# Optimization experiments

Measured on AMD Instinct MI355X. Metric: run time of the kernel, lower is better.

Reference implementation:

```python
import jax, jax.numpy as jnp
import numpy as np

B, S = 32, 4096
Q_DIM, KV_DIM, A_DIM = 512, 512, 128


def setup_inputs() -> dict:
    key = jax.random.key(0)
    k1, k2, k3, k4, k5, k6 = jax.random.split(key, 6)
    query = jax.random.normal(k1, (B, Q_DIM), dtype=jnp.float32)
    kv = jax.random.normal(k2, (B, S, KV_DIM), dtype=jnp.float32)
    mask = jax.random.randint(k3, (B, S), 0, 2).astype(bool)
    # learned params (torch Linear(in, out, bias=False) stores W as [out, in]; we apply x @ W.T)
    Wq = jax.random.normal(k4, (A_DIM, Q_DIM), dtype=jnp.float32) / np.sqrt(Q_DIM)
    Wk = jax.random.normal(k5, (A_DIM, KV_DIM), dtype=jnp.float32) / np.sqrt(KV_DIM)
    Ws = jax.random.normal(k6, (1, A_DIM), dtype=jnp.float32) / np.sqrt(A_DIM)
    return {"query": query, "kv": kv, "mask": mask, "Wq": Wq, "Wk": Wk, "Ws": Ws}


def reference(query, kv, mask, Wq, Wk, Ws):
    # q: [B, 1, A], k: [B, S, A]
    q = jnp.einsum('bq,aq->ba', query, Wq)[:, None, :]
    k = jnp.einsum('bsk,ak->bsa', kv, Wk)
    # additive (Bahdanau) scores: [B, S]
    scores = jnp.einsum('bsa,a->bs', jnp.tanh(q + k), Ws[0])
    scores = jnp.where(mask, scores, -jnp.inf)
    weights = jax.nn.softmax(scores, axis=-1)
    context = jnp.einsum('bs,bsk->bk', weights, kv)
    return context, weights
```

## Files before the change

### kernel.cpp

```cpp
#include <hip/hip_runtime.h>


typedef __attribute__((ext_vector_type(8))) short short8;
typedef __attribute__((ext_vector_type(4))) float f32x4;

#define S_LEN 4096
#define BATCH 32
#define KVD 512
#define AD 128
#define SCHN 32
#define CHUNKS_PER_B (S_LEN / SCHN)
#define NCHUNK (BATCH * CHUNKS_PER_B)

#define FLAG_OFF   0
#define Q_OFF      1024
#define WK_OFF     17408
#define SCORES_OFF 148480
#define MD_OFF     672768
#define CTXP_OFF   705536

__device__ __forceinline__ unsigned short f2bf(float f) {
  unsigned int u = __float_as_uint(f);
  u = (u + 0x7FFFu + ((u >> 16) & 1u)) >> 16;
  return (unsigned short)u;
}
__device__ __forceinline__ float tanh_fast(float x) {
  return 1.0f - 2.0f / (1.0f + __expf(2.0f * x));
}
__device__ __forceinline__ short8 pack8(float4 lo, float4 hi) {
  short8 r;
  r[0] = (short)f2bf(lo.x); r[1] = (short)f2bf(lo.y);
  r[2] = (short)f2bf(lo.z); r[3] = (short)f2bf(lo.w);
  r[4] = (short)f2bf(hi.x); r[5] = (short)f2bf(hi.y);
  r[6] = (short)f2bf(hi.z); r[7] = (short)f2bf(hi.w);
  return r;
}

__global__ __launch_bounds__(256) void prep_kernel(
    const float* __restrict__ query, const float* __restrict__ Wq,
    const float* __restrict__ Wk, const void* __restrict__ maskp,
    float* __restrict__ qws, unsigned short* __restrict__ wkb,
    int* __restrict__ flagp) {
  int blk = blockIdx.x, t = threadIdx.x;
  if (blk < 32) {
    __shared__ float qrow[KVD];
    qrow[t] = query[blk * KVD + t];
    qrow[t + 256] = query[blk * KVD + t + 256];
    __syncthreads();
    int a = t >> 1, half = t & 1;
    const float4* wq4 = (const float4*)(Wq + (size_t)a * KVD + half * 256);
    const float4* qr4 = (const float4*)(qrow + half * 256);
    float s = 0.f;
#pragma unroll 8
    for (int i = 0; i < 64; ++i) {
      float4 wv = wq4[i], qv = qr4[i];
      s += wv.x * qv.x + wv.y * qv.y + wv.z * qv.z + wv.w * qv.w;
    }
    s += __shfl_xor(s, 1);
    if (half == 0) qws[blk * AD + a] = s;
  } else if (blk < 40) {
    int j = blk - 32;
    const float4* src = (const float4*)Wk;
#pragma unroll 4
    for (int i = 0; i < 8; ++i) {
      int idx4 = j * 2048 + i * 256 + t;
      float4 v = src[idx4];
      ushort4 o;
      o.x = f2bf(v.x); o.y = f2bf(v.y); o.z = f2bf(v.z); o.w = f2bf(v.w);
      ((ushort4*)wkb)[idx4] = o;
    }
  } else {
    __shared__ int okv;
    if (t == 0) okv = 1;
    __syncthreads();
    if (t < 128) {
      int wv = ((const int*)maskp)[t];
      if (!(wv == 0 || wv == 1)) okv = 0;
    }
    __syncthreads();
    if (t == 0) flagp[0] = okv;
  }
}

__global__ __launch_bounds__(256, 3) void main_kernel(
    const float* __restrict__ kv, const void* __restrict__ maskp,
    const float* __restrict__ Ws, const float* __restrict__ qws,
    const unsigned short* __restrict__ wkb, const int* __restrict__ flagp,
    float* __restrict__ scores, float* __restrict__ md,
    float* __restrict__ ctxp) {
  int t = threadIdx.x;
  int lane = t & 63, wave = t >> 6;
  int g = blockIdx.x * 4 + wave;
  int b = g >> 7, chunk = g & 127;
  int s0 = chunk * SCHN;
  int lr = lane & 15, lg = lane >> 4;

  __shared__ float esc[4][SCHN];
  __shared__ float ssc[4][SCHN];

  const float* arow0 = kv + ((size_t)b * S_LEN + s0 + lr) * KVD + lg * 8;
  const float* arow1 = arow0 + (size_t)16 * KVD;
  const unsigned short* brow = wkb + (size_t)lr * KVD + lg * 8;

  f32x4 acc[2][8];
#pragma unroll
  for (int mi = 0; mi < 2; ++mi)
#pragma unroll
    for (int n = 0; n < 8; ++n) acc[mi][n] = (f32x4)0.f;

  for (int kk = 0; kk < KVD / 32; ++kk) {
    int ko = kk * 32;
    float4 a0lo = *(const float4*)(arow0 + ko);
    float4 a0hi = *(const float4*)(arow0 + ko + 4);
    float4 a1lo = *(const float4*)(arow1 + ko);
    float4 a1hi = *(const float4*)(arow1 + ko + 4);
    short8 bfr[8];
#pragma unroll
    for (int n = 0; n < 8; ++n)
      bfr[n] = *(const short8*)(brow + (size_t)n * 16 * KVD + ko);
    short8 af0 = pack8(a0lo, a0hi);
    short8 af1 = pack8(a1lo, a1hi);
#pragma unroll
    for (int n = 0; n < 8; ++n) {
      acc[0][n] = __builtin_amdgcn_mfma_f32_16x16x32_bf16(af0, bfr[n], acc[0][n], 0, 0, 0);
      acc[1][n] = __builtin_amdgcn_mfma_f32_16x16x32_bf16(af1, bfr[n], acc[1][n], 0, 0, 0);
    }
  }

  float qv[8], wv[8];
#pragma unroll
  for (int n = 0; n < 8; ++n) {
    qv[n] = qws[b * AD + n * 16 + lr];
    wv[n] = Ws[n * 16 + lr];
  }
  int flag = flagp[0];
  float sc[2][4];
#pragma unroll
  for (int mi = 0; mi < 2; ++mi) {
#pragma unroll
    for (int reg = 0; reg < 4; ++reg) {
      float v = 0.f;
#pragma unroll
      for (int n = 0; n < 8; ++n)
        v += tanh_fast(qv[n] + acc[mi][n][reg]) * wv[n];
      v += __shfl_xor(v, 1);
      v += __shfl_xor(v, 2);
      v += __shfl_xor(v, 4);
      v += __shfl_xor(v, 8);
      int gs = b * S_LEN + s0 + 16 * mi + 4 * lg + reg;
      int mk = flag ? ((const int*)maskp)[gs]
                    : (int)((const unsigned char*)maskp)[gs];
      sc[mi][reg] = mk ? v : -INFINITY;
    }
  }

  float m = -INFINITY;
#pragma unroll
  for (int mi = 0; mi < 2; ++mi)
#pragma unroll
    for (int reg = 0; reg < 4; ++reg) m = fmaxf(m, sc[mi][reg]);
  m = fmaxf(m, __shfl_xor(m, 16));
  m = fmaxf(m, __shfl_xor(m, 32));
  float e[2][4];
  float d = 0.f;
#pragma unroll
  for (int mi = 0; mi < 2; ++mi)
#pragma unroll
    for (int reg = 0; reg < 4; ++reg) {
      e[mi][reg] = (sc[mi][reg] == -INFINITY) ? 0.f : __expf(sc[mi][reg] - m);
      d += e[mi][reg];
    }
  d += __shfl_xor(d, 16);
  d += __shfl_xor(d, 32);

  if (lr == 0) {
#pragma unroll
    for (int mi = 0; mi < 2; ++mi)
#pragma unroll
      for (int reg = 0; reg < 4; ++reg) {
        int srow = 16 * mi + 4 * lg + reg;
        esc[wave][srow] = e[mi][reg];
        ssc[wave][srow] = sc[mi][reg];
      }
  }
  if (lane == 0) { md[g * 2] = m; md[g * 2 + 1] = d; }
  __syncthreads();

  if (lane < SCHN) scores[b * S_LEN + s0 + lane] = ssc[wave][lane];

  float4 c0 = make_float4(0.f, 0.f, 0.f, 0.f);
  float4 c1 = make_float4(0.f, 0.f, 0.f, 0.f);
  const float* kvc = kv + ((size_t)b * S_LEN + s0) * KVD + lane * 8;
#pragma unroll 4
  for (int s = 0; s < SCHN; ++s) {
    float ev = esc[wave][s];
    float4 v0 = *(const float4*)(kvc + (size_t)s * KVD);
    float4 v1 = *(const float4*)(kvc + (size_t)s * KVD + 4);
    c0.x += ev * v0.x; c0.y += ev * v0.y; c0.z += ev * v0.z; c0.w += ev * v0.w;
    c1.x += ev * v1.x; c1.y += ev * v1.y; c1.z += ev * v1.z; c1.w += ev * v1.w;
  }
  float* cp = ctxp + (size_t)g * KVD + lane * 8;
  *(float4*)cp = c0;
  *(float4*)(cp + 4) = c1;
}

__global__ __launch_bounds__(512) void combine_kernel(
    const float* __restrict__ md, const float* __restrict__ ctxp,
    const float* __restrict__ scores, float* __restrict__ out) {
  int b = blockIdx.x, t = threadIdx.x;
  __shared__ float mv[CHUNKS_PER_B], dv[CHUNKS_PER_B], scl[CHUNKS_PER_B];
  __shared__ float Msh, Dsh;
  if (t < CHUNKS_PER_B) {
    mv[t] = md[(b * CHUNKS_PER_B + t) * 2];
    dv[t] = md[(b * CHUNKS_PER_B + t) * 2 + 1];
  }
  __syncthreads();
  if (t < 64) {
    float m = fmaxf(mv[t], mv[t + 64]);
    m = fmaxf(m, __shfl_xor(m, 32));
    m = fmaxf(m, __shfl_xor(m, 16));
    m = fmaxf(m, __shfl_xor(m, 8));
    m = fmaxf(m, __shfl_xor(m, 4));
    m = fmaxf(m, __shfl_xor(m, 2));
    m = fmaxf(m, __shfl_xor(m, 1));
    if (t == 0) Msh = m;
  }
  __syncthreads();
  float M = Msh;
  if (t < CHUNKS_PER_B) scl[t] = (dv[t] > 0.f) ? __expf(mv[t] - M) : 0.f;
  __syncthreads();
  if (t < 64) {
    float d = scl[t] * dv[t] + scl[t + 64] * dv[t + 64];
    d += __shfl_xor(d, 32);
    d += __shfl_xor(d, 16);
    d += __shfl_xor(d, 8);
    d += __shfl_xor(d, 4);
    d += __shfl_xor(d, 2);
    d += __shfl_xor(d, 1);
    if (t == 0) Dsh = d;
  }
  __syncthreads();
  float invD = 1.f / Dsh;
  for (int c = t; c < KVD; c += 512) {
    float sum = 0.f;
#pragma unroll 4
    for (int j = 0; j < CHUNKS_PER_B; ++j)
      sum += scl[j] * ctxp[(size_t)(b * CHUNKS_PER_B + j) * KVD + c];
    out[b * KVD + c] = sum * invD;
  }
  for (int s = t; s < S_LEN; s += 512) {
    float sc = scores[b * S_LEN + s];
    out[BATCH * KVD + b * S_LEN + s] = __expf(sc - M) * invD;
  }
}

extern "C" void kernel_launch(void* const* d_in, const int* in_sizes, int n_in,
                              void* d_out, int out_size, void* d_ws, size_t ws_size,
                              hipStream_t stream) {
  const float* query = (const float*)d_in[0];
  const float* kv    = (const float*)d_in[1];
  const void*  maskp = d_in[2];
  const float* Wq    = (const float*)d_in[3];
  const float* Wk    = (const float*)d_in[4];
  const float* Ws    = (const float*)d_in[5];
  float* out = (float*)d_out;
  char* w = (char*)d_ws;
  int* flagp = (int*)(w + FLAG_OFF);
  float* qws = (float*)(w + Q_OFF);
  unsigned short* wkb = (unsigned short*)(w + WK_OFF);
  float* scores = (float*)(w + SCORES_OFF);
  float* md = (float*)(w + MD_OFF);
  float* ctxp = (float*)(w + CTXP_OFF);

  prep_kernel<<<41, 256, 0, stream>>>(query, Wq, Wk, maskp, qws, wkb, flagp);
  main_kernel<<<NCHUNK / 4, 256, 0, stream>>>(kv, maskp, Ws, qws, wkb, flagp,
                                              scores, md, ctxp);
  combine_kernel<<<BATCH, 512, 0, stream>>>(md, ctxp, scores, out);
}
```

Measured before the change: 144.7 us.

## Stage kv chunk once in LDS as bf16 and split combine into parallel stages

Each 64-thread block now loads its 32-row kv chunk from global memory once, converts it to bf16 and stores it in a swizzled LDS tile. Both the MFMA projection and the weighted context sum read from that tile, so kv is no longer read from global memory twice. The mask is preloaded per lane and broadcast with shuffles, and the combine step is split into a per-batch reduction kernel plus a wider 2D-grid kernel. The trade-offs are an extra kernel launch, 32 KB of LDS per one-wave block, and bf16 rounding of kv in the context sum, which loses accuracy compared with the fp32 sum.

```diff
diff --git a/kernel.cpp b/kernel.cpp
--- a/kernel.cpp
+++ b/kernel.cpp
@@ -18,22 +18,21 @@
 #define SCORES_OFF 148480
 #define MD_OFF     672768
 #define CTXP_OFF   705536
-
-__device__ __forceinline__ unsigned short f2bf(float f) {
+#define SCL_OFF    9094144
+#define MD2_OFF    9110528
+
+__device__ __forceinline__ unsigned short f2bf_rne(float f) {
   unsigned int u = __float_as_uint(f);
   u = (u + 0x7FFFu + ((u >> 16) & 1u)) >> 16;
   return (unsigned short)u;
 }
+__device__ __forceinline__ unsigned int packbf(float a, float b) {
+  unsigned int lo = __float_as_uint(a) + 0x8000u;
+  unsigned int hi = __float_as_uint(b) + 0x8000u;
+  return (lo >> 16) | (hi & 0xFFFF0000u);
+}
 __device__ __forceinline__ float tanh_fast(float x) {
   return 1.0f - 2.0f / (1.0f + __expf(2.0f * x));
-}
-__device__ __forceinline__ short8 pack8(float4 lo, float4 hi) {
-  short8 r;
-  r[0] = (short)f2bf(lo.x); r[1] = (short)f2bf(lo.y);
-  r[2] = (short)f2bf(lo.z); r[3] = (short)f2bf(lo.w);
-  r[4] = (short)f2bf(hi.x); r[5] = (short)f2bf(hi.y);
-  r[6] = (short)f2bf(hi.z); r[7] = (short)f2bf(hi.w);
-  return r;
 }
 
 __global__ __launch_bounds__(256) void prep_kernel(
@@ -66,7 +65,8 @@
       int idx4 = j * 2048 + i * 256 + t;
       float4 v = src[idx4];
       ushort4 o;
-      o.x = f2bf(v.x); o.y = f2bf(v.y); o.z = f2bf(v.z); o.w = f2bf(v.w);
+      o.x = f2bf_rne(v.x); o.y = f2bf_rne(v.y);
+      o.z = f2bf_rne(v.z); o.w = f2bf_rne(v.w);
       ((ushort4*)wkb)[idx4] = o;
     }
   } else {
@@ -82,58 +82,72 @@
   }
 }
 
-__global__ __launch_bounds__(256, 3) void main_kernel(
+__global__ __launch_bounds__(64) void main_kernel(
     const float* __restrict__ kv, const void* __restrict__ maskp,
     const float* __restrict__ Ws, const float* __restrict__ qws,
     const unsigned short* __restrict__ wkb, const int* __restrict__ flagp,
     float* __restrict__ scores, float* __restrict__ md,
     float* __restrict__ ctxp) {
-  int t = threadIdx.x;
-  int lane = t & 63, wave = t >> 6;
-  int g = blockIdx.x * 4 + wave;
-  int b = g >> 7, chunk = g & 127;
+  int lane = threadIdx.x;
+  int g = blockIdx.x;
+  int b = g >> 7, chunk = g & (CHUNKS_PER_B - 1);
   int s0 = chunk * SCHN;
   int lr = lane & 15, lg = lane >> 4;
 
-  __shared__ float esc[4][SCHN];
-  __shared__ float ssc[4][SCHN];
-
-  const float* arow0 = kv + ((size_t)b * S_LEN + s0 + lr) * KVD + lg * 8;
-  const float* arow1 = arow0 + (size_t)16 * KVD;
-  const unsigned short* brow = wkb + (size_t)lr * KVD + lg * 8;
-
-  f32x4 acc[2][8];
-#pragma unroll
-  for (int mi = 0; mi < 2; ++mi)
-#pragma unroll
-    for (int n = 0; n < 8; ++n) acc[mi][n] = (f32x4)0.f;
-
-  for (int kk = 0; kk < KVD / 32; ++kk) {
-    int ko = kk * 32;
-    float4 a0lo = *(const float4*)(arow0 + ko);
-    float4 a0hi = *(const float4*)(arow0 + ko + 4);
-    float4 a1lo = *(const float4*)(arow1 + ko);
-    float4 a1hi = *(const float4*)(arow1 + ko + 4);
-    short8 bfr[8];
-#pragma unroll
-    for (int n = 0; n < 8; ++n)
-      bfr[n] = *(const short8*)(brow + (size_t)n * 16 * KVD + ko);
-    short8 af0 = pack8(a0lo, a0hi);
-    short8 af1 = pack8(a1lo, a1hi);
-#pragma unroll
-    for (int n = 0; n < 8; ++n) {
-      acc[0][n] = __builtin_amdgcn_mfma_f32_16x16x32_bf16(af0, bfr[n], acc[0][n], 0, 0, 0);
-      acc[1][n] = __builtin_amdgcn_mfma_f32_16x16x32_bf16(af1, bfr[n], acc[1][n], 0, 0, 0);
-    }
-  }
-
+  __shared__ char tileb[SCHN * 1024];
+  __shared__ float escf[SCHN];
+
+  int flag = flagp[0];
+  int mload = 0;
+  if (lane < SCHN) {
+    int gs = b * S_LEN + s0 + lane;
+    mload = flag ? ((const int*)maskp)[gs]
+                 : (int)((const unsigned char*)maskp)[gs];
+  }
   float qv[8], wv[8];
 #pragma unroll
   for (int n = 0; n < 8; ++n) {
     qv[n] = qws[b * AD + n * 16 + lr];
     wv[n] = Ws[n * 16 + lr];
   }
-  int flag = flagp[0];
+
+  const float* src = kv + ((size_t)b * S_LEN + s0) * KVD;
+#pragma unroll 8
+  for (int r = 0; r < SCHN; ++r) {
+    float4 v0 = *(const float4*)(src + (size_t)r * KVD + lane * 4);
+    float4 v1 = *(const float4*)(src + (size_t)r * KVD + 256 + lane * 4);
+    uint2 w0, w1;
+    w0.x = packbf(v0.x, v0.y); w0.y = packbf(v0.z, v0.w);
+    w1.x = packbf(v1.x, v1.y); w1.y = packbf(v1.z, v1.w);
+    int xr = (r & 7) << 4;
+    *(uint2*)(tileb + ((r * 1024 + lane * 8) ^ xr)) = w0;
+    *(uint2*)(tileb + ((r * 1024 + 512 + lane * 8) ^ xr)) = w1;
+  }
+  __syncthreads();
+
+  f32x4 acc[2][8];
+#pragma unroll
+  for (int mi = 0; mi < 2; ++mi)
+#pragma unroll
+    for (int n = 0; n < 8; ++n) acc[mi][n] = (f32x4)0.f;
+
+  const unsigned short* brow = wkb + (size_t)lr * KVD + lg * 8;
+  const char* ta0 = tileb + lr * 1024;
+  const char* ta1 = tileb + (16 + lr) * 1024;
+  int axor = (lr & 7) << 4;
+
+  for (int kk = 0; kk < KVD / 32; ++kk) {
+    int ko = (kk * 64 + lg * 16) ^ axor;
+    short8 af0 = *(const short8*)(ta0 + ko);
+    short8 af1 = *(const short8*)(ta1 + ko);
+#pragma unroll
+    for (int n = 0; n < 8; ++n) {
+      short8 bf = *(const short8*)(brow + (size_t)n * 16 * KVD + kk * 32);
+      acc[0][n] = __builtin_amdgcn_mfma_f32_16x16x32_bf16(af0, bf, acc[0][n], 0, 0, 0);
+      acc[1][n] = __builtin_amdgcn_mfma_f32_16x16x32_bf16(af1, bf, acc[1][n], 0, 0, 0);
+    }
+  }
+
   float sc[2][4];
 #pragma unroll
   for (int mi = 0; mi < 2; ++mi) {
@@ -147,9 +161,8 @@
       v += __shfl_xor(v, 2);
       v += __shfl_xor(v, 4);
       v += __shfl_xor(v, 8);
-      int gs = b * S_LEN + s0 + 16 * mi + 4 * lg + reg;
-      int mk = flag ? ((const int*)maskp)[gs]
-                    : (int)((const unsigned char*)maskp)[gs];
+      int row = 16 * mi + 4 * lg + reg;
+      int mk = __shfl(mload, row);
       sc[mi][reg] = mk ? v : -INFINITY;
     }
   }
@@ -178,79 +191,93 @@
     for (int mi = 0; mi < 2; ++mi)
 #pragma unroll
       for (int reg = 0; reg < 4; ++reg) {
-        int srow = 16 * mi + 4 * lg + reg;
-        esc[wave][srow] = e[mi][reg];
-        ssc[wave][srow] = sc[mi][reg];
+        int row = 16 * mi + 4 * lg + reg;
+        escf[row] = e[mi][reg];
+        scores[b * S_LEN + s0 + row] = sc[mi][reg];
       }
   }
   if (lane == 0) { md[g * 2] = m; md[g * 2 + 1] = d; }
   __syncthreads();
 
-  if (lane < SCHN) scores[b * S_LEN + s0 + lane] = ssc[wave][lane];
-
   float4 c0 = make_float4(0.f, 0.f, 0.f, 0.f);
   float4 c1 = make_float4(0.f, 0.f, 0.f, 0.f);
-  const float* kvc = kv + ((size_t)b * S_LEN + s0) * KVD + lane * 8;
 #pragma unroll 4
   for (int s = 0; s < SCHN; ++s) {
-    float ev = esc[wave][s];
-    float4 v0 = *(const float4*)(kvc + (size_t)s * KVD);
-    float4 v1 = *(const float4*)(kvc + (size_t)s * KVD + 4);
-    c0.x += ev * v0.x; c0.y += ev * v0.y; c0.z += ev * v0.z; c0.w += ev * v0.w;
-    c1.x += ev * v1.x; c1.y += ev * v1.y; c1.z += ev * v1.z; c1.w += ev * v1.w;
+    float ev = escf[s];
+    uint4 u = *(const uint4*)(tileb + ((s * 1024 + lane * 16) ^ ((s & 7) << 4)));
+    c0.x += ev * __uint_as_float(u.x << 16);
+    c0.y += ev * __uint_as_float(u.x & 0xFFFF0000u);
+    c0.z += ev * __uint_as_float(u.y << 16);
+    c0.w += ev * __uint_as_float(u.y & 0xFFFF0000u);
+    c1.x += ev * __uint_as_float(u.z << 16);
+    c1.y += ev * __uint_as_float(u.z & 0xFFFF0000u);
+    c1.z += ev * __uint_as_float(u.w << 16);
+    c1.w += ev * __uint_as_float(u.w & 0xFFFF0000u);
   }
   float* cp = ctxp + (size_t)g * KVD + lane * 8;
   *(float4*)cp = c0;
   *(float4*)(cp + 4) = c1;
 }
 
-__global__ __launch_bounds__(512) void combine_kernel(
-    const float* __restrict__ md, const float* __restrict__ ctxp,
-    const float* __restrict__ scores, float* __restrict__ out) {
+__global__ __launch_bounds__(128) void combineA_kernel(
+    const float* __restrict__ md, float* __restrict__ scl,
+    float* __restrict__ md2) {
   int b = blockIdx.x, t = threadIdx.x;
-  __shared__ float mv[CHUNKS_PER_B], dv[CHUNKS_PER_B], scl[CHUNKS_PER_B];
-  __shared__ float Msh, Dsh;
-  if (t < CHUNKS_PER_B) {
-    mv[t] = md[(b * CHUNKS_PER_B + t) * 2];
-    dv[t] = md[(b * CHUNKS_PER_B + t) * 2 + 1];
-  }
+  float mv = md[(b * CHUNKS_PER_B + t) * 2];
+  float dv = md[(b * CHUNKS_PER_B + t) * 2 + 1];
+  __shared__ float rmax[2], rsum[2];
+  float m = mv;
+  m = fmaxf(m, __shfl_xor(m, 1));
+  m = fmaxf(m, __shfl_xor(m, 2));
+  m = fmaxf(m, __shfl_xor(m, 4));
+  m = fmaxf(m, __shfl_xor(m, 8));
+  m = fmaxf(m, __shfl_xor(m, 16));
+  m = fmaxf(m, __shfl_xor(m, 32));
+  if ((t & 63) == 0) rmax[t >> 6] = m;
   __syncthreads();
-  if (t < 64) {
-    float m = fmaxf(mv[t], mv[t + 64]);
-    m = fmaxf(m, __shfl_xor(m, 32));
-    m = fmaxf(m, __shfl_xor(m, 16));
-    m = fmaxf(m, __shfl_xor(m, 8));
-    m = fmaxf(m, __shfl_xor(m, 4));
-    m = fmaxf(m, __shfl_xor(m, 2));
-    m = fmaxf(m, __shfl_xor(m, 1));
-    if (t == 0) Msh = m;
-  }
+  float M = fmaxf(rmax[0], rmax[1]);
+  float e = (dv > 0.f) ? __expf(mv - M) : 0.f;
+  float pd = e * dv;
+  pd += __shfl_xor(pd, 1);
+  pd += __shfl_xor(pd, 2);
+  pd += __shfl_xor(pd, 4);
+  pd += __shfl_xor(pd, 8);
+  pd += __shfl_xor(pd, 16);
+  pd += __shfl_xor(pd, 32);
+  if ((t & 63) == 0) rsum[t >> 6] = pd;
   __syncthreads();
-  float M = Msh;
-  if (t < CHUNKS_PER_B) scl[t] = (dv[t] > 0.f) ? __expf(mv[t] - M) : 0.f;
-  __syncthreads();
-  if (t < 64) {
-    float d = scl[t] * dv[t] + scl[t + 64] * dv[t + 64];
-    d += __shfl_xor(d, 32);
-    d += __shfl_xor(d, 16);
-    d += __shfl_xor(d, 8);
-    d += __shfl_xor(d, 4);
-    d += __shfl_xor(d, 2);
-    d += __shfl_xor(d, 1);
-    if (t == 0) Dsh = d;
-  }
-  __syncthreads();
-  float invD = 1.f / Dsh;
-  for (int c = t; c < KVD; c += 512) {
+  float D = rsum[0] + rsum[1];
+  float invD = 1.f / D;
+  scl[b * CHUNKS_PER_B + t] = e * invD;
+  if (t == 0) { md2[b * 2] = M; md2[b * 2 + 1] = invD; }
+}
+
+__global__ __launch_bounds__(256) void combineB_kernel(
+    const float* __restrict__ scl, const float* __restrict__ md2,
+    const float* __restrict__ ctxp, const float* __restrict__ scores,
+    float* __restrict__ out) {
+  int strip = blockIdx.x, b = blockIdx.y, t = threadIdx.x;
+  if (strip < 8) {
+    __shared__ float part[4][64];
+    int c = strip * 64 + (t & 63);
+    int jg = t >> 6;
     float sum = 0.f;
-#pragma unroll 4
-    for (int j = 0; j < CHUNKS_PER_B; ++j)
-      sum += scl[j] * ctxp[(size_t)(b * CHUNKS_PER_B + j) * KVD + c];
-    out[b * KVD + c] = sum * invD;
-  }
-  for (int s = t; s < S_LEN; s += 512) {
-    float sc = scores[b * S_LEN + s];
-    out[BATCH * KVD + b * S_LEN + s] = __expf(sc - M) * invD;
+    for (int j = jg; j < CHUNKS_PER_B; j += 4)
+      sum += scl[b * CHUNKS_PER_B + j] *
+             ctxp[(size_t)(b * CHUNKS_PER_B + j) * KVD + c];
+    part[jg][t & 63] = sum;
+    __syncthreads();
+    if (t < 64)
+      out[b * KVD + c] = part[0][t] + part[1][t] + part[2][t] + part[3][t];
+  } else {
+    float M = md2[b * 2], invD = md2[b * 2 + 1];
+    int sbase = (strip - 8) * 1024;
+#pragma unroll
+    for (int i = 0; i < 4; ++i) {
+      int s = sbase + i * 256 + t;
+      float scv = scores[b * S_LEN + s];
+      out[BATCH * KVD + b * S_LEN + s] = __expf(scv - M) * invD;
+    }
   }
 }
 
@@ -271,9 +298,12 @@
   float* scores = (float*)(w + SCORES_OFF);
   float* md = (float*)(w + MD_OFF);
   float* ctxp = (float*)(w + CTXP_OFF);
+  float* scl = (float*)(w + SCL_OFF);
+  float* md2 = (float*)(w + MD2_OFF);
 
   prep_kernel<<<41, 256, 0, stream>>>(query, Wq, Wk, maskp, qws, wkb, flagp);
-  main_kernel<<<NCHUNK / 4, 256, 0, stream>>>(kv, maskp, Ws, qws, wkb, flagp,
-                                              scores, md, ctxp);
-  combine_kernel<<<BATCH, 512, 0, stream>>>(md, ctxp, scores, out);
-}
+  main_kernel<<<NCHUNK, 64, 0, stream>>>(kv, maskp, Ws, qws, wkb, flagp,
+                                         scores, md, ctxp);
+  combineA_kernel<<<BATCH, 128, 0, stream>>>(md, scl, md2);
+  combineB_kernel<<<dim3(12, BATCH), 256, 0, stream>>>(scl, md2, ctxp, scores, out);
+}
```

Result: faster. 134.9 us (-6.8%).
